# Kernel tuning notes

Measured on AMD Instinct MI355X. Metric: run time of the kernel, lower is better.

## Reference

```python
import jax, jax.numpy as jnp
import numpy as np

H = 1024
E = 8
K = 2
N = 16384
LN_EPS = 1e-5


def _layernorm(h, g, b):
    m = jnp.mean(h, axis=-1, keepdims=True)
    v = jnp.mean(jnp.square(h - m), axis=-1, keepdims=True)
    return (h - m) * jax.lax.rsqrt(v + LN_EPS) * g + b


def setup_inputs() -> dict:
    key = jax.random.key(0)
    ks = jax.random.split(key, 8)
    s = 0.02
    return {
        "x": jax.random.normal(ks[0], (N, H), dtype=jnp.float32),
        "Wg": jax.random.normal(ks[1], (H, E), dtype=jnp.float32) * s,
        "bg": jnp.zeros((E,), dtype=jnp.float32),
        "W1": jax.random.normal(ks[2], (E, H, H), dtype=jnp.float32) * s,
        "b1": jnp.zeros((E, H), dtype=jnp.float32),
        "g1": jnp.ones((E, H), dtype=jnp.float32),
        "be1": jnp.zeros((E, H), dtype=jnp.float32),
        "W2": jax.random.normal(ks[3], (E, H, H), dtype=jnp.float32) * s,
        "b2": jnp.zeros((E, H), dtype=jnp.float32),
        "g2": jnp.ones((E, H), dtype=jnp.float32),
        "be2": jnp.zeros((E, H), dtype=jnp.float32),
    }


def reference(x, Wg, bg, W1, b1, g1, be1, W2, b2, g2, be2):
    # Gating: softmax over experts, top-k, renormalize
    gate_probs = jax.nn.softmax(x @ Wg + bg, axis=1)            # [N, E]
    tk_p, tk_i = jax.lax.top_k(gate_probs, K)                    # [N, K]
    tk_p = tk_p / (jnp.sum(tk_p, axis=1, keepdims=True) + 1e-9)
    # Dense per-expert combine weight (zero where expert not selected)
    w = jnp.sum(tk_p[:, :, None] * jax.nn.one_hot(tk_i, E, dtype=x.dtype), axis=1)  # [N, E]

    # ResidualBlock per expert, computed densely for all tokens (dropout = eval/no-op)
    h = jnp.einsum('nh,eho->eno', x, W1) + b1[:, None, :]        # [E, N, H]
    h = jax.nn.relu(_layernorm(h, g1[:, None, :], be1[:, None, :]))
    h = jnp.einsum('enh,eho->eno', h, W2) + b2[:, None, :]
    h = _layernorm(h, g2[:, None, :], be2[:, None, :])
    y = jax.nn.relu(x[None, :, :] + h)                           # [E, N, H]

    moe_out = jnp.einsum('ne,enh->nh', w, y)                     # [N, H]
    return moe_out, gate_probs
```

## Files before the change

kernel.cpp:

```cpp
#include <hip/hip_runtime.h>
#include <cstdint>
#include <cstddef>

constexpr int H_DIM = 1024;
constexpr int NE    = 8;
constexpr int NT    = 16384;
constexpr int NP    = NT * 2;

constexpr int BM = 256, BN = 256, BK = 64;
constexpr int NKT = H_DIM / BK;
constexpr int MAX_WG = NE * (NT / BM) * (H_DIM / BN);

typedef __attribute__((ext_vector_type(8))) short          short8;
typedef __attribute__((ext_vector_type(8))) unsigned short ushort8;
typedef __attribute__((ext_vector_type(4))) float          f32x4;

__device__ __forceinline__ unsigned short f2bf(float f) {
  union { float f; uint32_t u; } c; c.f = f;
  uint32_t u = c.u;
  u = (u + 0x7fffu + ((u >> 16) & 1u)) >> 16;
  return (unsigned short)u;
}
__device__ __forceinline__ float bf2f(unsigned short h) {
  union { uint32_t u; float f; } c; c.u = ((uint32_t)h) << 16;
  return c.f;
}

__device__ __forceinline__ void gload16(const unsigned short* g, unsigned short* l) {
  __builtin_amdgcn_global_load_lds((const __attribute__((address_space(1))) void*)g,
                                   (__attribute__((address_space(3))) void*)l, 16, 0, 0);
}

__global__ __launch_bounds__(256) void transpose_convert_kernel(
    const float* __restrict__ W1, const float* __restrict__ W2,
    unsigned short* __restrict__ T1, unsigned short* __restrict__ T2)
{
  __shared__ float tile[64][65];
  int zi = blockIdx.z;
  const float* W = (zi < 8) ? W1 : W2;
  unsigned short* T = (zi < 8) ? T1 : T2;
  int e  = zi & 7;
  int o0 = blockIdx.x * 64;
  int h0 = blockIdx.y * 64;
  int c  = threadIdx.x & 63;
  int r0 = (threadIdx.x >> 6) * 16;
  const float* src = W + ((size_t)e * H_DIM + h0) * H_DIM + o0;
#pragma unroll
  for (int i = 0; i < 16; ++i)
    tile[r0 + i][c] = src[(size_t)(r0 + i) * H_DIM + c];
  __syncthreads();
  unsigned short* dst = T + ((size_t)e * H_DIM + o0) * H_DIM + h0;
#pragma unroll
  for (int i = 0; i < 16; ++i)
    dst[(size_t)(r0 + i) * H_DIM + c] = f2bf(tile[c][r0 + i]);
}

__global__ __launch_bounds__(256) void xgate_kernel(
    const float* __restrict__ X, const float* __restrict__ Wg,
    const float* __restrict__ bg, unsigned short* __restrict__ Xb,
    float* __restrict__ gate_out, int* __restrict__ tk_e, float* __restrict__ tk_w)
{
  int wid = threadIdx.x >> 6, lane = threadIdx.x & 63;
  int n = blockIdx.x * 4 + wid;
  const float* xr = X + (size_t)n * H_DIM;

  const float4* xp = (const float4*)(xr + lane * 16);
  float4 f0 = xp[0], f1 = xp[1], f2 = xp[2], f3 = xp[3];
  float v[16] = {f0.x,f0.y,f0.z,f0.w, f1.x,f1.y,f1.z,f1.w,
                 f2.x,f2.y,f2.z,f2.w, f3.x,f3.y,f3.z,f3.w};

  ushort8 u0, u1;
#pragma unroll
  for (int j = 0; j < 8; ++j) { u0[j] = f2bf(v[j]); u1[j] = f2bf(v[8 + j]); }
  ushort8* xb = (ushort8*)(Xb + (size_t)n * H_DIM + lane * 16);
  xb[0] = u0; xb[1] = u1;

  float acc[8];
#pragma unroll
  for (int e = 0; e < 8; ++e) acc[e] = 0.f;
#pragma unroll
  for (int j = 0; j < 16; ++j) {
    int h = lane * 16 + j;
    const float4* wg = (const float4*)(Wg + (size_t)h * 8);
    float4 a = wg[0], b = wg[1];
    float xv = v[j];
    acc[0] += xv * a.x; acc[1] += xv * a.y; acc[2] += xv * a.z; acc[3] += xv * a.w;
    acc[4] += xv * b.x; acc[5] += xv * b.y; acc[6] += xv * b.z; acc[7] += xv * b.w;
  }
#pragma unroll
  for (int m = 1; m < 64; m <<= 1) {
#pragma unroll
    for (int e = 0; e < 8; ++e) acc[e] += __shfl_xor(acc[e], m);
  }
#pragma unroll
  for (int e = 0; e < 8; ++e) acc[e] += bg[e];

  float mx = acc[0];
#pragma unroll
  for (int e = 1; e < 8; ++e) mx = fmaxf(mx, acc[e]);
  float g[8], s = 0.f;
#pragma unroll
  for (int e = 0; e < 8; ++e) { g[e] = __expf(acc[e] - mx); s += g[e]; }
  float inv = 1.f / s;
#pragma unroll
  for (int e = 0; e < 8; ++e) g[e] *= inv;

  int e0 = 0; float b0 = g[0];
#pragma unroll
  for (int e = 1; e < 8; ++e) if (g[e] > b0) { b0 = g[e]; e0 = e; }
  int e1 = -1; float b1v = -1.f;
#pragma unroll
  for (int e = 0; e < 8; ++e) if (e != e0 && g[e] > b1v) { b1v = g[e]; e1 = e; }
  float s2 = b0 + b1v + 1e-9f;

  if (lane == 0) {
    float4* gp = (float4*)(gate_out + (size_t)n * 8);
    gp[0] = make_float4(g[0], g[1], g[2], g[3]);
    gp[1] = make_float4(g[4], g[5], g[6], g[7]);
    tk_e[2 * n] = e0; tk_e[2 * n + 1] = e1;
    tk_w[2 * n] = b0 / s2; tk_w[2 * n + 1] = b1v / s2;
  }
}

__global__ __launch_bounds__(256) void hist_kernel(
    const int* __restrict__ tk_e, int* __restrict__ blockHist)
{
  __shared__ int h[8];
  if (threadIdx.x < 8) h[threadIdx.x] = 0;
  __syncthreads();
  int i0 = blockIdx.x * 512 + threadIdx.x;
  atomicAdd(&h[tk_e[i0]], 1);
  atomicAdd(&h[tk_e[i0 + 256]], 1);
  __syncthreads();
  if (threadIdx.x < 8) blockHist[blockIdx.x * 8 + threadIdx.x] = h[threadIdx.x];
}

__global__ void scan_kernel(const int* __restrict__ blockHist,
                            int* __restrict__ blockBase,
                            int* __restrict__ count, int* __restrict__ offs)
{
  int e = threadIdx.x;
  if (e < 8) {
    int run = 0;
    for (int b = 0; b < 64; ++b) { blockBase[b * 8 + e] = run; run += blockHist[b * 8 + e]; }
    count[e] = run;
  }
  __syncthreads();
  if (threadIdx.x == 0) {
    int o = 0;
    for (int k = 0; k < 8; ++k) { offs[k] = o; o += count[k]; }
  }
  __syncthreads();
  if (e < 8) {
    int o = offs[e];
    for (int b = 0; b < 64; ++b) blockBase[b * 8 + e] += o;
  }
}

__global__ __launch_bounds__(256) void place_kernel(
    const int* __restrict__ tk_e, const int* __restrict__ blockBase,
    int* __restrict__ pairTok, int* __restrict__ pairExp, int* __restrict__ slots)
{
  __shared__ int cur[8];
  if (threadIdx.x < 8) cur[threadIdx.x] = blockBase[blockIdx.x * 8 + threadIdx.x];
  __syncthreads();
#pragma unroll
  for (int j = 0; j < 2; ++j) {
    int i = blockIdx.x * 512 + j * 256 + threadIdx.x;
    int e = tk_e[i];
    int s = atomicAdd(&cur[e], 1);
    pairTok[s] = i >> 1; pairExp[s] = e; slots[i] = s;
  }
}

__global__ void worklist_kernel(const int* __restrict__ count,
                                int* __restrict__ wl, int* __restrict__ wlCount)
{
  __shared__ int nmt[8], ebase[8], totalS;
  if (threadIdx.x == 0) {
    int o = 0;
    for (int e = 0; e < 8; ++e) {
      nmt[e] = (count[e] + BM - 1) / BM;
      ebase[e] = o;
      o += nmt[e] * (H_DIM / BN);
    }
    totalS = o;
    wlCount[0] = o;
  }
  __syncthreads();
  int total = totalS;
  for (int i = threadIdx.x; i < total; i += blockDim.x) {
    int e = 0;
    while (e < 7 && i >= ebase[e + 1]) ++e;
    int loc = i - ebase[e];
    int nt = loc / nmt[e];
    int mt = loc - nt * nmt[e];
    wl[i] = (e << 20) | (nt << 16) | mt;
  }
}

template<bool GATHER>
__global__ __launch_bounds__(512, 2) void gemm8_kernel(
    const unsigned short* __restrict__ Ab,
    const unsigned short* __restrict__ Bt,
    const float* __restrict__ bias,
    const int* __restrict__ pairTok,
    const int* __restrict__ count, const int* __restrict__ offs,
    const int* __restrict__ wl, const int* __restrict__ wlCount,
    unsigned short* __restrict__ Out)
{
  __shared__ unsigned short As[2 * 2 * 8192];
  __shared__ unsigned short Bs[2 * 2 * 8192];

  const int total = wlCount[0];
  const int orig = blockIdx.x;
  if (orig >= total) return;
  const int qq = total >> 3, rr = total & 7;
  const int xcd = orig & 7, sub = orig >> 3;
  const int idx = (xcd < rr ? xcd * (qq + 1) : rr * (qq + 1) + (xcd - rr) * qq) + sub;
  const int ent = wl[idx];
  const int e = ent >> 20, ntb = (ent >> 16) & 15, mtb = ent & 0xffff;
  const int cnt = count[e], base = offs[e];

  const int tid = threadIdx.x;
  const int wid = tid >> 6, l = tid & 63;
  const int wr = wid >> 2, wc = wid & 3;

  const int rih0 = (((tid >> 6)) >> 1) * 16 + ((tid >> 2) & 15);
  const int rih1 = ((8 + (tid >> 6)) >> 1) * 16 + ((tid >> 2) & 15);
  const int selem = ((tid >> 6) & 1) * 32 + (((tid & 3) * 8) ^ (((tid >> 5) & 1) << 4));

  const unsigned short* ap[4];
  const unsigned short* bp[4];
  {
    int g0 = mtb * 256 + rih0;       if (g0 >= cnt) g0 = cnt - 1;
    int g1 = mtb * 256 + rih1;       if (g1 >= cnt) g1 = cnt - 1;
    int g2 = mtb * 256 + 128 + rih0; if (g2 >= cnt) g2 = cnt - 1;
    int g3 = mtb * 256 + 128 + rih1; if (g3 >= cnt) g3 = cnt - 1;
    size_t r0, r1, r2, r3;
    if (GATHER) {
      r0 = (size_t)pairTok[base + g0]; r1 = (size_t)pairTok[base + g1];
      r2 = (size_t)pairTok[base + g2]; r3 = (size_t)pairTok[base + g3];
    } else {
      r0 = (size_t)(base + g0); r1 = (size_t)(base + g1);
      r2 = (size_t)(base + g2); r3 = (size_t)(base + g3);
    }
    ap[0] = Ab + r0 * H_DIM + selem;
    ap[1] = Ab + r1 * H_DIM + selem;
    ap[2] = Ab + r2 * H_DIM + selem;
    ap[3] = Ab + r3 * H_DIM + selem;
    const unsigned short* bbase = Bt + ((size_t)e * H_DIM + ntb * 256) * H_DIM + selem;
    bp[0] = bbase + (size_t)(rih0)       * H_DIM;
    bp[1] = bbase + (size_t)(rih1)       * H_DIM;
    bp[2] = bbase + (size_t)(128 + rih0) * H_DIM;
    bp[3] = bbase + (size_t)(128 + rih1) * H_DIM;
  }

#define A_DST(t, h, i) (As + ((t) & 1) * 16384 + (h) * 8192 + (i) * 4096 + wid * 512)
#define B_DST(t, h, i) (Bs + ((t) & 1) * 16384 + (h) * 8192 + (i) * 4096 + wid * 512)

  const int loff = ((l & 15) * 64 + (l >> 4) * 16) ^ (((l >> 3) & 1) << 5);
  const char* AsB = (const char*)As + wr * 16384 + loff;
  const char* BsB = (const char*)Bs + (wc >> 1) * 16384 + loff;
  const int bsub = (wc & 1) * 4;

  gload16(ap[0], A_DST(0, 0, 0)); gload16(ap[1], A_DST(0, 0, 1));
  gload16(ap[2], A_DST(0, 1, 0)); gload16(ap[3], A_DST(0, 1, 1));
  gload16(bp[0], B_DST(0, 0, 0)); gload16(bp[1], B_DST(0, 0, 1));
  gload16(bp[2], B_DST(0, 1, 0)); gload16(bp[3], B_DST(0, 1, 1));
  gload16(bp[0] + BK, B_DST(1, 0, 0)); gload16(bp[1] + BK, B_DST(1, 0, 1));
  gload16(bp[2] + BK, B_DST(1, 1, 0)); gload16(bp[3] + BK, B_DST(1, 1, 1));
  asm volatile("s_waitcnt vmcnt(4)" ::: "memory");
  __builtin_amdgcn_s_barrier();

  f32x4 acc[8][4] = {};

  for (int t = 0; t < NKT; ++t) {
    const int db = t & 1;
    const int dboff = db * 32768;
    short8 bfrag[4][2];
#pragma unroll
    for (int q = 0; q < 4; ++q) {
      short8 af[2][2];
#pragma unroll
      for (int j = 0; j < 2; ++j)
#pragma unroll
        for (int ks = 0; ks < 2; ++ks)
          af[j][ks] = *(const short8*)(AsB + dboff + ((q * 2 + j) * 2 + ks) * 1024);
      if (q == 0) {
#pragma unroll
        for (int r = 0; r < 4; ++r)
#pragma unroll
          for (int ks = 0; ks < 2; ++ks)
            bfrag[r][ks] = *(const short8*)(BsB + dboff + ((bsub + r) * 2 + ks) * 1024);
      }
      if (q == 0 && t + 1 < NKT) {
        gload16(ap[0] + (t + 1) * BK, A_DST(t + 1, 0, 0));
        gload16(ap[1] + (t + 1) * BK, A_DST(t + 1, 0, 1));
      }
      if (q == 1 && t + 1 < NKT) {
        gload16(ap[2] + (t + 1) * BK, A_DST(t + 1, 1, 0));
        gload16(ap[3] + (t + 1) * BK, A_DST(t + 1, 1, 1));
      }
      if (q == 2 && t + 2 < NKT) {
        gload16(bp[0] + (t + 2) * BK, B_DST(t + 2, 0, 0));
        gload16(bp[1] + (t + 2) * BK, B_DST(t + 2, 0, 1));
      }
      if (q == 3 && t + 2 < NKT) {
        gload16(bp[2] + (t + 2) * BK, B_DST(t + 2, 1, 0));
        gload16(bp[3] + (t + 2) * BK, B_DST(t + 2, 1, 1));
      }
      __builtin_amdgcn_s_barrier();
      __builtin_amdgcn_s_setprio(1);
#pragma unroll
      for (int j = 0; j < 2; ++j)
#pragma unroll
        for (int r = 0; r < 4; ++r)
#pragma unroll
          for (int ks = 0; ks < 2; ++ks)
            acc[q * 2 + j][r] = __builtin_amdgcn_mfma_f32_16x16x32_bf16(
                af[j][ks], bfrag[r][ks], acc[q * 2 + j][r], 0, 0, 0);
      __builtin_amdgcn_s_setprio(0);
      if (q == 3) {
        if (t + 2 < NKT) asm volatile("s_waitcnt vmcnt(4)" ::: "memory");
        else             asm volatile("s_waitcnt vmcnt(0)" ::: "memory");
      }
      __builtin_amdgcn_s_barrier();
    }
  }

  float bvv[4];
#pragma unroll
  for (int r = 0; r < 4; ++r)
    bvv[r] = bias[e * H_DIM + ntb * 256 + wc * 64 + r * 16 + (l & 15)];
#pragma unroll
  for (int j = 0; j < 8; ++j) {
    int grow0 = mtb * 256 + wr * 128 + j * 16 + (l >> 4) * 4;
#pragma unroll
    for (int r = 0; r < 4; ++r) {
      int gcol = ntb * 256 + wc * 64 + r * 16 + (l & 15);
#pragma unroll
      for (int v = 0; v < 4; ++v) {
        int row = grow0 + v;
        if (row < cnt)
          Out[(size_t)(base + row) * H_DIM + gcol] = f2bf(acc[j][r][v] + bvv[r]);
      }
    }
  }
#undef A_DST
#undef B_DST
}

__global__ __launch_bounds__(256) void ln_relu_kernel(
    unsigned short* __restrict__ buf, const float* __restrict__ gamma,
    const float* __restrict__ beta, const int* __restrict__ pairExp)
{
  int wid = threadIdx.x >> 6, lane = threadIdx.x & 63;
  int row = blockIdx.x * 4 + wid;
  int e = pairExp[row];
  unsigned short* r = buf + (size_t)row * H_DIM;
  ushort8 u0 = ((const ushort8*)r)[lane];
  ushort8 u1 = ((const ushort8*)r)[lane + 64];
  float v[16];
#pragma unroll
  for (int j = 0; j < 8; ++j) { v[j] = bf2f(u0[j]); v[8 + j] = bf2f(u1[j]); }
  float s = 0.f, ss = 0.f;
#pragma unroll
  for (int j = 0; j < 16; ++j) { s += v[j]; ss += v[j] * v[j]; }
#pragma unroll
  for (int m = 1; m < 64; m <<= 1) { s += __shfl_xor(s, m); ss += __shfl_xor(ss, m); }
  float mean = s * (1.f / 1024.f);
  float var  = ss * (1.f / 1024.f) - mean * mean;
  float rs   = rsqrtf(var + 1e-5f);

  int h0 = lane * 8, h1 = 512 + lane * 8;
  const float4* gp0 = (const float4*)(gamma + (size_t)e * H_DIM + h0);
  const float4* bp0 = (const float4*)(beta  + (size_t)e * H_DIM + h0);
  const float4* gp1 = (const float4*)(gamma + (size_t)e * H_DIM + h1);
  const float4* bp1 = (const float4*)(beta  + (size_t)e * H_DIM + h1);
  float4 ga = gp0[0], gb = gp0[1], gc = gp1[0], gd = gp1[1];
  float4 ba = bp0[0], bb = bp0[1], bc = bp1[0], bd = bp1[1];
  float gv[16] = {ga.x,ga.y,ga.z,ga.w, gb.x,gb.y,gb.z,gb.w,
                  gc.x,gc.y,gc.z,gc.w, gd.x,gd.y,gd.z,gd.w};
  float bv[16] = {ba.x,ba.y,ba.z,ba.w, bb.x,bb.y,bb.z,bb.w,
                  bc.x,bc.y,bc.z,bc.w, bd.x,bd.y,bd.z,bd.w};
#pragma unroll
  for (int j = 0; j < 8; ++j) {
    float t0 = fmaxf((v[j]     - mean) * rs * gv[j]     + bv[j],     0.f);
    float t1 = fmaxf((v[8 + j] - mean) * rs * gv[8 + j] + bv[8 + j], 0.f);
    u0[j] = f2bf(t0); u1[j] = f2bf(t1);
  }
  ((ushort8*)r)[lane] = u0; ((ushort8*)r)[lane + 64] = u1;
}

__global__ __launch_bounds__(256) void combine_kernel(
    const unsigned short* __restrict__ buf2, const float* __restrict__ X,
    const float* __restrict__ g2, const float* __restrict__ be2,
    const int* __restrict__ slots, const int* __restrict__ tk_e,
    const float* __restrict__ tk_w, float* __restrict__ out)
{
  int wid = threadIdx.x >> 6, lane = threadIdx.x & 63;
  int n = blockIdx.x * 4 + wid;
  int h0 = lane * 8, h1 = 512 + lane * 8;

  const float4* xp0 = (const float4*)(X + (size_t)n * H_DIM + h0);
  const float4* xp1 = (const float4*)(X + (size_t)n * H_DIM + h1);
  float4 xa = xp0[0], xb = xp0[1], xc = xp1[0], xd = xp1[1];
  float xv[16] = {xa.x,xa.y,xa.z,xa.w, xb.x,xb.y,xb.z,xb.w,
                  xc.x,xc.y,xc.z,xc.w, xd.x,xd.y,xd.z,xd.w};
  float o[16];
#pragma unroll
  for (int j = 0; j < 16; ++j) o[j] = 0.f;

#pragma unroll
  for (int k = 0; k < 2; ++k) {
    int slot = slots[2 * n + k];
    int e = tk_e[2 * n + k];
    float w = tk_w[2 * n + k];
    const unsigned short* r = buf2 + (size_t)slot * H_DIM;
    ushort8 u0 = ((const ushort8*)r)[lane];
    ushort8 u1 = ((const ushort8*)r)[lane + 64];
    float v[16];
#pragma unroll
    for (int j = 0; j < 8; ++j) { v[j] = bf2f(u0[j]); v[8 + j] = bf2f(u1[j]); }
    float s = 0.f, ss = 0.f;
#pragma unroll
    for (int j = 0; j < 16; ++j) { s += v[j]; ss += v[j] * v[j]; }
#pragma unroll
    for (int m = 1; m < 64; m <<= 1) { s += __shfl_xor(s, m); ss += __shfl_xor(ss, m); }
    float mean = s * (1.f / 1024.f);
    float var  = ss * (1.f / 1024.f) - mean * mean;
    float rs   = rsqrtf(var + 1e-5f);

    const float4* gp0 = (const float4*)(g2  + (size_t)e * H_DIM + h0);
    const float4* bp0 = (const float4*)(be2 + (size_t)e * H_DIM + h0);
    const float4* gp1 = (const float4*)(g2  + (size_t)e * H_DIM + h1);
    const float4* bp1 = (const float4*)(be2 + (size_t)e * H_DIM + h1);
    float4 ga = gp0[0], gb = gp0[1], gc = gp1[0], gd = gp1[1];
    float4 ba = bp0[0], bb = bp0[1], bc = bp1[0], bd = bp1[1];
    float gv[16] = {ga.x,ga.y,ga.z,ga.w, gb.x,gb.y,gb.z,gb.w,
                    gc.x,gc.y,gc.z,gc.w, gd.x,gd.y,gd.z,gd.w};
    float bvv[16] = {ba.x,ba.y,ba.z,ba.w, bb.x,bb.y,bb.z,bb.w,
                     bc.x,bc.y,bc.z,bc.w, bd.x,bd.y,bd.z,bd.w};
#pragma unroll
    for (int j = 0; j < 16; ++j) {
      float u = (v[j] - mean) * rs * gv[j] + bvv[j];
      float y = fmaxf(xv[j] + u, 0.f);
      o[j] += w * y;
    }
  }

  float4* op0 = (float4*)(out + (size_t)n * H_DIM + h0);
  float4* op1 = (float4*)(out + (size_t)n * H_DIM + h1);
  op0[0] = make_float4(o[0], o[1], o[2], o[3]);
  op0[1] = make_float4(o[4], o[5], o[6], o[7]);
  op1[0] = make_float4(o[8], o[9], o[10], o[11]);
  op1[1] = make_float4(o[12], o[13], o[14], o[15]);
}

extern "C" void kernel_launch(void* const* d_in, const int* in_sizes, int n_in,
                              void* d_out, int out_size, void* d_ws, size_t ws_size,
                              hipStream_t stream)
{
  const float* x   = (const float*)d_in[0];
  const float* Wg  = (const float*)d_in[1];
  const float* bg  = (const float*)d_in[2];
  const float* W1  = (const float*)d_in[3];
  const float* b1  = (const float*)d_in[4];
  const float* g1  = (const float*)d_in[5];
  const float* be1 = (const float*)d_in[6];
  const float* W2  = (const float*)d_in[7];
  const float* b2  = (const float*)d_in[8];
  const float* g2  = (const float*)d_in[9];
  const float* be2 = (const float*)d_in[10];
  float* out = (float*)d_out;
  float* gate_out = out + (size_t)NT * H_DIM;

  char* ws = (char*)d_ws;
  size_t off = 0;
  auto alloc = [&](size_t bytes) { char* p = ws + off; off += (bytes + 255) & ~(size_t)255; return p; };
  unsigned short* w1bt = (unsigned short*)alloc((size_t)NE * H_DIM * H_DIM * 2);
  unsigned short* w2bt = (unsigned short*)alloc((size_t)NE * H_DIM * H_DIM * 2);
  unsigned short* buf1 = (unsigned short*)alloc((size_t)NP * H_DIM * 2);
  unsigned short* buf2 = (unsigned short*)alloc((size_t)NP * H_DIM * 2);
  int*   tk_e      = (int*)alloc((size_t)NP * 4);
  float* tk_w      = (float*)alloc((size_t)NP * 4);
  int*   pairTok   = (int*)alloc((size_t)NP * 4);
  int*   pairExp   = (int*)alloc((size_t)NP * 4);
  int*   slots     = (int*)alloc((size_t)NP * 4);
  int*   blockHist = (int*)alloc(64 * 8 * 4);
  int*   blockBase = (int*)alloc(64 * 8 * 4);
  int*   count     = (int*)alloc(8 * 4);
  int*   offs      = (int*)alloc(8 * 4);
  int*   wl        = (int*)alloc(MAX_WG * 4);
  int*   wlCount   = (int*)alloc(4);
  (void)in_sizes; (void)n_in; (void)out_size; (void)ws_size;

  unsigned short* Xb = buf2;

  transpose_convert_kernel<<<dim3(16, 16, 16), 256, 0, stream>>>(W1, W2, w1bt, w2bt);
  xgate_kernel<<<dim3(NT / 4), 256, 0, stream>>>(x, Wg, bg, Xb, gate_out, tk_e, tk_w);
  hist_kernel<<<dim3(64), 256, 0, stream>>>(tk_e, blockHist);
  scan_kernel<<<dim3(1), 64, 0, stream>>>(blockHist, blockBase, count, offs);
  worklist_kernel<<<dim3(1), 256, 0, stream>>>(count, wl, wlCount);
  place_kernel<<<dim3(64), 256, 0, stream>>>(tk_e, blockBase, pairTok, pairExp, slots);
  gemm8_kernel<true><<<dim3(MAX_WG), 512, 0, stream>>>(
      Xb, w1bt, b1, pairTok, count, offs, wl, wlCount, buf1);
  ln_relu_kernel<<<dim3(NP / 4), 256, 0, stream>>>(buf1, g1, be1, pairExp);
  gemm8_kernel<false><<<dim3(MAX_WG), 512, 0, stream>>>(
      buf1, w2bt, b2, pairTok, count, offs, wl, wlCount, buf2);
  combine_kernel<<<dim3(NT / 4), 256, 0, stream>>>(
      buf2, x, g2, be2, slots, tk_e, tk_w, out);
}
```

Measured before the change: 413.4 us.

## Restructure expert GEMM into 4-stage BK=32 pipeline with one barrier per step

The grouped expert GEMM now uses a K-tile of 32 instead of 64 and a 4-slot shared-memory ring with prefetch three tiles ahead, replacing the 2-slot scheme with per-quarter staggered loads. Each iteration loads all A/B fragments at once, issues 32 MFMAs, and syncs with a single barrier instead of eight per 64-wide K tile. The aim is to cut barrier overhead and deepen latency hiding while keeping the same LDS footprint. In exchange, per-iteration MFMA work is halved and more fragment registers stay live at once, which may hurt occupancy or issue overlap.

```diff
diff --git a/kernel.cpp b/kernel.cpp
--- a/kernel.cpp
+++ b/kernel.cpp
@@ -7,7 +7,7 @@
 constexpr int NT    = 16384;
 constexpr int NP    = NT * 2;
 
-constexpr int BM = 256, BN = 256, BK = 64;
+constexpr int BM = 256, BN = 256, BK = 32;
 constexpr int NKT = H_DIM / BK;
 constexpr int MAX_WG = NE * (NT / BM) * (H_DIM / BN);
 
@@ -200,7 +200,7 @@
 }
 
 template<bool GATHER>
-__global__ __launch_bounds__(512, 2) void gemm8_kernel(
+__global__ __launch_bounds__(512, 2) void gemm4_kernel(
     const unsigned short* __restrict__ Ab,
     const unsigned short* __restrict__ Bt,
     const float* __restrict__ bias,
@@ -209,8 +209,8 @@
     const int* __restrict__ wl, const int* __restrict__ wlCount,
     unsigned short* __restrict__ Out)
 {
-  __shared__ unsigned short As[2 * 2 * 8192];
-  __shared__ unsigned short Bs[2 * 2 * 8192];
+  __shared__ unsigned short As[4 * 8192];
+  __shared__ unsigned short Bs[4 * 8192];
 
   const int total = wlCount[0];
   const int orig = blockIdx.x;
@@ -226,107 +226,69 @@
   const int wid = tid >> 6, l = tid & 63;
   const int wr = wid >> 2, wc = wid & 3;
 
-  const int rih0 = (((tid >> 6)) >> 1) * 16 + ((tid >> 2) & 15);
-  const int rih1 = ((8 + (tid >> 6)) >> 1) * 16 + ((tid >> 2) & 15);
-  const int selem = ((tid >> 6) & 1) * 32 + (((tid & 3) * 8) ^ (((tid >> 5) & 1) << 4));
-
-  const unsigned short* ap[4];
-  const unsigned short* bp[4];
+  const int rsub = (l >> 2);
+  const int kswz = ((l & 3) * 8) ^ (((l >> 5) & 1) << 4);
+
+  const unsigned short *apg0, *apg1, *bpg0, *bpg1;
   {
-    int g0 = mtb * 256 + rih0;       if (g0 >= cnt) g0 = cnt - 1;
-    int g1 = mtb * 256 + rih1;       if (g1 >= cnt) g1 = cnt - 1;
-    int g2 = mtb * 256 + 128 + rih0; if (g2 >= cnt) g2 = cnt - 1;
-    int g3 = mtb * 256 + 128 + rih1; if (g3 >= cnt) g3 = cnt - 1;
-    size_t r0, r1, r2, r3;
-    if (GATHER) {
-      r0 = (size_t)pairTok[base + g0]; r1 = (size_t)pairTok[base + g1];
-      r2 = (size_t)pairTok[base + g2]; r3 = (size_t)pairTok[base + g3];
-    } else {
-      r0 = (size_t)(base + g0); r1 = (size_t)(base + g1);
-      r2 = (size_t)(base + g2); r3 = (size_t)(base + g3);
-    }
-    ap[0] = Ab + r0 * H_DIM + selem;
-    ap[1] = Ab + r1 * H_DIM + selem;
-    ap[2] = Ab + r2 * H_DIM + selem;
-    ap[3] = Ab + r3 * H_DIM + selem;
-    const unsigned short* bbase = Bt + ((size_t)e * H_DIM + ntb * 256) * H_DIM + selem;
-    bp[0] = bbase + (size_t)(rih0)       * H_DIM;
-    bp[1] = bbase + (size_t)(rih1)       * H_DIM;
-    bp[2] = bbase + (size_t)(128 + rih0) * H_DIM;
-    bp[3] = bbase + (size_t)(128 + rih1) * H_DIM;
-  }
-
-#define A_DST(t, h, i) (As + ((t) & 1) * 16384 + (h) * 8192 + (i) * 4096 + wid * 512)
-#define B_DST(t, h, i) (Bs + ((t) & 1) * 16384 + (h) * 8192 + (i) * 4096 + wid * 512)
+    int r0 = wid * 16 + rsub;
+    int r1 = 128 + wid * 16 + rsub;
+    int g0 = mtb * 256 + r0; if (g0 >= cnt) g0 = cnt - 1;
+    int g1 = mtb * 256 + r1; if (g1 >= cnt) g1 = cnt - 1;
+    size_t a0, a1;
+    if (GATHER) { a0 = (size_t)pairTok[base + g0]; a1 = (size_t)pairTok[base + g1]; }
+    else        { a0 = (size_t)(base + g0);        a1 = (size_t)(base + g1); }
+    apg0 = Ab + a0 * H_DIM + kswz;
+    apg1 = Ab + a1 * H_DIM + kswz;
+    const unsigned short* bb = Bt + ((size_t)e * H_DIM + ntb * 256) * H_DIM + kswz;
+    bpg0 = bb + (size_t)r0 * H_DIM;
+    bpg1 = bb + (size_t)r1 * H_DIM;
+  }
 
   const int loff = ((l & 15) * 64 + (l >> 4) * 16) ^ (((l >> 3) & 1) << 5);
-  const char* AsB = (const char*)As + wr * 16384 + loff;
-  const char* BsB = (const char*)Bs + (wc >> 1) * 16384 + loff;
-  const int bsub = (wc & 1) * 4;
-
-  gload16(ap[0], A_DST(0, 0, 0)); gload16(ap[1], A_DST(0, 0, 1));
-  gload16(ap[2], A_DST(0, 1, 0)); gload16(ap[3], A_DST(0, 1, 1));
-  gload16(bp[0], B_DST(0, 0, 0)); gload16(bp[1], B_DST(0, 0, 1));
-  gload16(bp[2], B_DST(0, 1, 0)); gload16(bp[3], B_DST(0, 1, 1));
-  gload16(bp[0] + BK, B_DST(1, 0, 0)); gload16(bp[1] + BK, B_DST(1, 0, 1));
-  gload16(bp[2] + BK, B_DST(1, 1, 0)); gload16(bp[3] + BK, B_DST(1, 1, 1));
-  asm volatile("s_waitcnt vmcnt(4)" ::: "memory");
+
+  auto STAGE = [&](int u) {
+    int sl = u & 3;
+    unsigned short* ad = As + sl * 8192 + wid * 512;
+    unsigned short* bd = Bs + sl * 8192 + wid * 512;
+    gload16(apg0 + (size_t)u * BK, ad);
+    gload16(apg1 + (size_t)u * BK, ad + 4096);
+    gload16(bpg0 + (size_t)u * BK, bd);
+    gload16(bpg1 + (size_t)u * BK, bd + 4096);
+  };
+
+  STAGE(0); STAGE(1); STAGE(2);
+  asm volatile("s_waitcnt vmcnt(8)" ::: "memory");
   __builtin_amdgcn_s_barrier();
 
   f32x4 acc[8][4] = {};
 
+#pragma unroll 4
   for (int t = 0; t < NKT; ++t) {
-    const int db = t & 1;
-    const int dboff = db * 32768;
-    short8 bfrag[4][2];
-#pragma unroll
-    for (int q = 0; q < 4; ++q) {
-      short8 af[2][2];
-#pragma unroll
-      for (int j = 0; j < 2; ++j)
-#pragma unroll
-        for (int ks = 0; ks < 2; ++ks)
-          af[j][ks] = *(const short8*)(AsB + dboff + ((q * 2 + j) * 2 + ks) * 1024);
-      if (q == 0) {
-#pragma unroll
-        for (int r = 0; r < 4; ++r)
-#pragma unroll
-          for (int ks = 0; ks < 2; ++ks)
-            bfrag[r][ks] = *(const short8*)(BsB + dboff + ((bsub + r) * 2 + ks) * 1024);
-      }
-      if (q == 0 && t + 1 < NKT) {
-        gload16(ap[0] + (t + 1) * BK, A_DST(t + 1, 0, 0));
-        gload16(ap[1] + (t + 1) * BK, A_DST(t + 1, 0, 1));
-      }
-      if (q == 1 && t + 1 < NKT) {
-        gload16(ap[2] + (t + 1) * BK, A_DST(t + 1, 1, 0));
-        gload16(ap[3] + (t + 1) * BK, A_DST(t + 1, 1, 1));
-      }
-      if (q == 2 && t + 2 < NKT) {
-        gload16(bp[0] + (t + 2) * BK, B_DST(t + 2, 0, 0));
-        gload16(bp[1] + (t + 2) * BK, B_DST(t + 2, 0, 1));
-      }
-      if (q == 3 && t + 2 < NKT) {
-        gload16(bp[2] + (t + 2) * BK, B_DST(t + 2, 1, 0));
-        gload16(bp[3] + (t + 2) * BK, B_DST(t + 2, 1, 1));
-      }
-      __builtin_amdgcn_s_barrier();
-      __builtin_amdgcn_s_setprio(1);
-#pragma unroll
-      for (int j = 0; j < 2; ++j)
-#pragma unroll
-        for (int r = 0; r < 4; ++r)
-#pragma unroll
-          for (int ks = 0; ks < 2; ++ks)
-            acc[q * 2 + j][r] = __builtin_amdgcn_mfma_f32_16x16x32_bf16(
-                af[j][ks], bfrag[r][ks], acc[q * 2 + j][r], 0, 0, 0);
-      __builtin_amdgcn_s_setprio(0);
-      if (q == 3) {
-        if (t + 2 < NKT) asm volatile("s_waitcnt vmcnt(4)" ::: "memory");
-        else             asm volatile("s_waitcnt vmcnt(0)" ::: "memory");
-      }
-      __builtin_amdgcn_s_barrier();
-    }
+    const int sl = t & 3;
+    const char* aB = (const char*)As + sl * 16384 + wr * 8192 + loff;
+    const char* bB = (const char*)Bs + sl * 16384 + wc * 4096 + loff;
+
+    short8 af[8], bfr[4];
+#pragma unroll
+    for (int j = 0; j < 8; ++j) af[j] = *(const short8*)(aB + j * 1024);
+#pragma unroll
+    for (int r = 0; r < 4; ++r) bfr[r] = *(const short8*)(bB + r * 1024);
+
+    if (t <= NKT - 4) STAGE(t + 3);
+
+    __builtin_amdgcn_s_setprio(1);
+#pragma unroll
+    for (int j = 0; j < 8; ++j)
+#pragma unroll
+      for (int r = 0; r < 4; ++r)
+        acc[j][r] = __builtin_amdgcn_mfma_f32_16x16x32_bf16(af[j], bfr[r], acc[j][r], 0, 0, 0);
+    __builtin_amdgcn_s_setprio(0);
+
+    if (t <= NKT - 4)      asm volatile("s_waitcnt vmcnt(8)" ::: "memory");
+    else if (t == NKT - 3) asm volatile("s_waitcnt vmcnt(4)" ::: "memory");
+    else if (t == NKT - 2) asm volatile("s_waitcnt vmcnt(0)" ::: "memory");
+    __builtin_amdgcn_s_barrier();
   }
 
   float bvv[4];
@@ -347,8 +309,6 @@
       }
     }
   }
-#undef A_DST
-#undef B_DST
 }
 
 __global__ __launch_bounds__(256) void ln_relu_kernel(
@@ -504,10 +464,10 @@
   scan_kernel<<<dim3(1), 64, 0, stream>>>(blockHist, blockBase, count, offs);
   worklist_kernel<<<dim3(1), 256, 0, stream>>>(count, wl, wlCount);
   place_kernel<<<dim3(64), 256, 0, stream>>>(tk_e, blockBase, pairTok, pairExp, slots);
-  gemm8_kernel<true><<<dim3(MAX_WG), 512, 0, stream>>>(
+  gemm4_kernel<true><<<dim3(MAX_WG), 512, 0, stream>>>(
       Xb, w1bt, b1, pairTok, count, offs, wl, wlCount, buf1);
   ln_relu_kernel<<<dim3(NP / 4), 256, 0, stream>>>(buf1, g1, be1, pairExp);
-  gemm8_kernel<false><<<dim3(MAX_WG), 512, 0, stream>>>(
+  gemm4_kernel<false><<<dim3(MAX_WG), 512, 0, stream>>>(
       buf1, w2bt, b2, pairTok, count, offs, wl, wlCount, buf2);
   combine_kernel<<<dim3(NT / 4), 256, 0, stream>>>(
       buf2, x, g2, be2, slots, tk_e, tk_w, out);
```

New measurement: 368.1 us. 11.0% less time.
